# Kernel tuning notes

Hardware: AMD Instinct MI355X
Metric: run time of the kernel (lower is better)

Reference implementation:

```python
import jax, jax.numpy as jnp
import numpy as np

E, H, K = 8, 256, 2        # num_experts, hidden_size, top-k
B, S, TD, ID = 16, 1024, 768, 1024
EPS = 1e-5

def gelu(x):
    return jax.nn.gelu(x, approximate=False)  # torch nn.GELU default = exact erf

def layer_norm(x, g, b):
    m = jnp.mean(x, axis=-1, keepdims=True)
    v = jnp.var(x, axis=-1, keepdims=True)
    return (x - m) * jax.lax.rsqrt(v + EPS) * g + b

def moe(x, gate_W, gate_b, W1, b1, W2, b2):
    # x: [B,S,H]
    gates = jax.nn.softmax(x @ gate_W + gate_b, axis=-1)        # [B,S,E]
    topv, topi = jax.lax.top_k(gates, K)                        # [B,S,K]
    # dense all-expert compute (faithful to the torch loop+stack)
    h = gelu(jnp.einsum('bsh,ehg->bseg', x, W1) + b1)           # [B,S,E,H]
    eo = jnp.einsum('bseg,egh->bseh', h, W2) + b2               # [B,S,E,H]
    sel = jnp.take_along_axis(eo, topi[..., None], axis=2)      # [B,S,K,H]
    return jnp.sum(sel * topv[..., None], axis=2)               # [B,S,H]

def setup_inputs() -> dict:
    key = jax.random.key(0)
    ks = jax.random.split(key, 12)
    def n(k, shape, scale=0.05):
        return jax.random.normal(k, shape, jnp.float32) * scale
    return dict(
        x=jax.random.normal(ks[0], (B, S, TD), jnp.float32),
        We=n(ks[1], (TD, H)), be=jnp.zeros((H,), jnp.float32),
        l2_emb=n(ks[2], (H,)), cl_emb=n(ks[3], (H,)),
        gate_W=n(ks[4], (H, E)), gate_b=jnp.zeros((E,), jnp.float32),
        W1=n(ks[5], (E, H, H)), b1=jnp.zeros((E, H), jnp.float32),
        W2=n(ks[6], (E, H, H)), b2=jnp.zeros((E, H), jnp.float32),
        l2_g=jnp.ones((H,), jnp.float32), l2_b=jnp.zeros((H,), jnp.float32),
        cl_g=jnp.ones((H,), jnp.float32), cl_b=jnp.zeros((H,), jnp.float32),
        Wt2i=n(ks[7], (H, ID)), bt2i=jnp.zeros((ID,), jnp.float32),
        Wcl=n(ks[8], (H, H)), bcl=jnp.zeros((H,), jnp.float32),
    )

def reference(x, We, be, l2_emb, cl_emb, gate_W, gate_b, W1, b1, W2, b2,
              l2_g, l2_b, cl_g, cl_b, Wt2i, bt2i, Wcl, bcl):
    # task == 'text2image'
    x = gelu(x @ We + be)                                       # text_embed + gelu
    l2_in = x + l2_emb
    cl_in = x + cl_emb
    l2 = gelu(layer_norm(moe(l2_in, gate_W, gate_b, W1, b1, W2, b2), l2_g, l2_b)) + l2_in
    cl = gelu(layer_norm(moe(cl_in, gate_W, gate_b, W1, b1, W2, b2), cl_g, cl_b)) + cl_in
    l2_res = l2 @ Wt2i + bt2i                                   # text_to_image head
    cl_res = cl @ Wcl + bcl                                     # cl_text_to_image head
    return (l2_res, cl_res)
```

## Files before the change

### kernel.cpp

```cpp
#include <hip/hip_runtime.h>
#include <hip/hip_bf16.h>
#include <math.h>

typedef __bf16 bf16_t;
typedef __bf16 bf16x4 __attribute__((ext_vector_type(4)));
typedef __bf16 bf16x8 __attribute__((ext_vector_type(8)));
typedef float  f32x4  __attribute__((ext_vector_type(4)));

#define NTOK 16384
#define HD   256
#define TD   768
#define ID   1024
#define NPAIR 32768
#define MOE_TPB 520
#define FLAG_CAP 4096

__device__ inline float fast_erf(float x){
    float ax = fabsf(x);
    float t = 1.0f / (1.0f + 0.3275911f*ax);
    float y = t*(0.254829592f + t*(-0.284496736f + t*(1.421413741f +
              t*(-1.453152027f + t*1.061405429f))));
    float e = 1.0f - y*__expf(-ax*ax);
    return copysignf(e, x);
}
__device__ inline float gelu_f(float x){
    return 0.5f * x * (1.0f + fast_erf(x * 0.70710678118654752f));
}
__device__ inline bf16x4 cvt4(float4 a){
    bf16x4 o; o[0]=(bf16_t)a.x; o[1]=(bf16_t)a.y; o[2]=(bf16_t)a.z; o[3]=(bf16_t)a.w; return o;
}
__device__ inline f32x4 mfma16(bf16x8 a, bf16x8 b, f32x4 c){
    return __builtin_amdgcn_mfma_f32_16x16x32_bf16(a, b, c, 0, 0, 0);
}

__global__ void k_zero(int* meta){
    if (threadIdx.x < 64) meta[threadIdx.x] = 0;
}

__global__ __launch_bounds__(256) void k_convert(
    const float* __restrict__ We, const float* __restrict__ W1,
    const float* __restrict__ W2, const float* __restrict__ Wt,
    const float* __restrict__ Wc,
    bf16_t* __restrict__ WeHi, bf16_t* __restrict__ WeLo,
    bf16_t* __restrict__ W1T,
    bf16_t* __restrict__ W2T, bf16_t* __restrict__ WtT, bf16_t* __restrict__ WcT)
{
    int idx = blockIdx.x*256 + threadIdx.x;
    if (idx < 196608){ int n=idx/768, k=idx%768; float f = We[k*256+n];
        bf16_t h = (bf16_t)f; WeHi[idx] = h; WeLo[idx] = (bf16_t)(f - (float)h); return; }
    idx -= 196608;
    if (idx < 524288){ int e=idx>>16, r=idx&65535, n=r>>8, k=r&255;
        W1T[(e<<16)+(n<<8)+k] = (bf16_t)W1[(e<<16)+(k<<8)+n]; return; }
    idx -= 524288;
    if (idx < 524288){ int e=idx>>16, r=idx&65535, n=r>>8, k=r&255;
        W2T[(e<<16)+(n<<8)+k] = (bf16_t)W2[(e<<16)+(k<<8)+n]; return; }
    idx -= 524288;
    if (idx < 262144){ int n=idx>>8, k=idx&255; WtT[idx] = (bf16_t)Wt[k*1024+n]; return; }
    idx -= 262144;
    if (idx < 65536){ int n=idx>>8, k=idx&255; WcT[idx] = (bf16_t)Wc[k*256+n]; return; }
}

__global__ __launch_bounds__(256) void k_embed(
    const float* __restrict__ x, const bf16_t* __restrict__ WeHi,
    const bf16_t* __restrict__ WeLo,
    const float* __restrict__ be, const float* __restrict__ l2e,
    const float* __restrict__ cle,
    float* __restrict__ l2f, float* __restrict__ clf)
{
    __shared__ bf16_t Ah[128][40];
    __shared__ bf16_t Al[128][40];
    __shared__ bf16_t Bh[64][40];
    __shared__ bf16_t Bl[64][40];
    int row0 = blockIdx.x*128, col0 = blockIdx.y*64;
    int t = threadIdx.x, wave = t>>6, lane = t&63;
    int wm = wave>>1, wn = wave&1;
    f32x4 acc[4][2] = {};
    for (int k0 = 0; k0 < TD; k0 += 32){
        __syncthreads();
        #pragma unroll
        for (int u=0; u<4; ++u){
            int fi = u*256 + t, r = fi>>3, q = fi&7;
            float4 v = *(const float4*)(x + (size_t)(row0+r)*TD + k0 + q*4);
            bf16x4 h = cvt4(v);
            float4 rl;
            rl.x = v.x-(float)h[0]; rl.y = v.y-(float)h[1];
            rl.z = v.z-(float)h[2]; rl.w = v.w-(float)h[3];
            *(bf16x4*)(&Ah[r][q*4]) = h;
            *(bf16x4*)(&Al[r][q*4]) = cvt4(rl);
        }
        {
            int r = t>>2, q = t&3;
            *(bf16x8*)(&Bh[r][q*8]) = *(const bf16x8*)(WeHi + (size_t)(col0+r)*TD + k0 + q*8);
            *(bf16x8*)(&Bl[r][q*8]) = *(const bf16x8*)(WeLo + (size_t)(col0+r)*TD + k0 + q*8);
        }
        __syncthreads();
        int kq = lane>>4, lr = lane&15;
        bf16x8 ah[4], al[4], bh[2], bl[2];
        #pragma unroll
        for (int m=0;m<4;++m){
            ah[m] = *(const bf16x8*)(&Ah[wm*64 + m*16 + lr][kq*8]);
            al[m] = *(const bf16x8*)(&Al[wm*64 + m*16 + lr][kq*8]);
        }
        #pragma unroll
        for (int n=0;n<2;++n){
            bh[n] = *(const bf16x8*)(&Bh[wn*32 + n*16 + lr][kq*8]);
            bl[n] = *(const bf16x8*)(&Bl[wn*32 + n*16 + lr][kq*8]);
        }
        #pragma unroll
        for (int m=0;m<4;++m)
            #pragma unroll
            for (int n=0;n<2;++n){
                acc[m][n] = mfma16(ah[m], bh[n], acc[m][n]);
                acc[m][n] = mfma16(ah[m], bl[n], acc[m][n]);
                acc[m][n] = mfma16(al[m], bh[n], acc[m][n]);
            }
    }
    int kq = lane>>4, lr = lane&15;
    #pragma unroll
    for (int n=0;n<2;++n){
        int col = col0 + wn*32 + n*16 + lr;
        float bv = be[col], lv = l2e[col], cv = cle[col];
        #pragma unroll
        for (int m=0;m<4;++m)
            #pragma unroll
            for (int r=0;r<4;++r){
                int row = row0 + wm*64 + m*16 + kq*4 + r;
                float v = gelu_f(acc[m][n][r] + bv);
                l2f[(size_t)row*HD + col] = v + lv;
                clf[(size_t)row*HD + col] = v + cv;
            }
    }
}

__global__ __launch_bounds__(256) void k_gate(
    const float* __restrict__ l2f, const float* __restrict__ clf,
    const float* __restrict__ gW, const float* __restrict__ gb,
    float* __restrict__ topv, int* __restrict__ topi,
    int* __restrict__ flaglist, int* __restrict__ nflag,
    bf16_t* __restrict__ l2h, bf16_t* __restrict__ clh)
{
    __shared__ float gw[2048];
    int t = threadIdx.x;
    for (int i=t; i<2048; i+=256) gw[i] = gW[i];
    __syncthreads();
    int wave = t>>6, lane = t&63;
    int idx = blockIdx.x*4 + wave;
    int br = idx>>14, tok = idx&16383;
    const float* in = br ? clf : l2f;
    float4 v = *(const float4*)(in + (size_t)tok*HD + lane*4);
    float xv[4] = {v.x, v.y, v.z, v.w};
    {
        bf16x4 hv; hv[0]=(bf16_t)v.x; hv[1]=(bf16_t)v.y; hv[2]=(bf16_t)v.z; hv[3]=(bf16_t)v.w;
        bf16_t* hout = br ? clh : l2h;
        *(bf16x4*)(hout + (size_t)tok*HD + lane*4) = hv;
    }
    float p[8];
    #pragma unroll
    for (int e=0;e<8;++e) p[e] = 0.f;
    #pragma unroll
    for (int j=0;j<4;++j){
        const float* g = &gw[(lane*4+j)*8];
        #pragma unroll
        for (int e=0;e<8;++e) p[e] += xv[j]*g[e];
    }
    #pragma unroll
    for (int e=0;e<8;++e){
        float s = p[e];
        #pragma unroll
        for (int o=32;o>0;o>>=1) s += __shfl_xor(s, o);
        p[e] = s + gb[e];
    }
    float mx = p[0];
    #pragma unroll
    for (int e=1;e<8;++e) mx = fmaxf(mx, p[e]);
    float den = 0.f;
    #pragma unroll
    for (int e=0;e<8;++e) den += expf(p[e]-mx);
    int i1 = 0; float m1 = p[0];
    #pragma unroll
    for (int e=1;e<8;++e) if (p[e] > m1){ m1 = p[e]; i1 = e; }
    int i2 = (i1==0)?1:0; float m2 = p[i2];
    #pragma unroll
    for (int e=0;e<8;++e) if (e != i1 && p[e] > m2){ m2 = p[e]; i2 = e; }
    if (lane == 0){
        topv[idx*2]   = expf(m1-mx)/den;
        topv[idx*2+1] = expf(m2-mx)/den;
        topi[idx*2]   = i1;
        topi[idx*2+1] = i2;
        float m3 = -1e30f;
        #pragma unroll
        for (int e=0;e<8;++e) if (e != i1 && e != i2) m3 = fmaxf(m3, p[e]);
        if (m2 - m3 < 1e-3f){
            int slot = atomicAdd(nflag, 1);
            if (slot < FLAG_CAP) flaglist[slot] = idx;
        }
    }
}

__global__ __launch_bounds__(256) void k_refine(
    const float* __restrict__ x, const float* __restrict__ We,
    const float* __restrict__ be,
    const float* __restrict__ l2e, const float* __restrict__ cle,
    const float* __restrict__ gW, const float* __restrict__ gb,
    const int* __restrict__ flaglist, const int* __restrict__ nflag,
    float* __restrict__ topv, int* __restrict__ topi)
{
    __shared__ float xs[768];
    __shared__ double red[256][8];
    int t = threadIdx.x;
    int nf = *nflag; if (nf > FLAG_CAP) nf = FLAG_CAP;
    for (int f = blockIdx.x; f < nf; f += gridDim.x){
        int idx = flaglist[f];
        int br = idx>>14, tok = idx&16383;
        __syncthreads();
        for (int i=t; i<768; i+=256) xs[i] = x[(size_t)tok*768 + i];
        __syncthreads();
        double u = 0.0;
        for (int j=0;j<768;++j) u += (double)xs[j] * (double)We[(size_t)j*256 + t];
        u += (double)be[t];
        double act = 0.5*u*(1.0 + erf(u*0.70710678118654752440));
        double li = act + (double)(br ? cle[t] : l2e[t]);
        #pragma unroll
        for (int e=0;e<8;++e) red[t][e] = li * (double)gW[t*8+e];
        __syncthreads();
        for (int s=128; s>0; s>>=1){
            if (t < s){
                #pragma unroll
                for (int e=0;e<8;++e) red[t][e] += red[t+s][e];
            }
            __syncthreads();
        }
        if (t == 0){
            double p[8];
            #pragma unroll
            for (int e=0;e<8;++e) p[e] = red[0][e] + (double)gb[e];
            int i1 = 0; double m1 = p[0];
            #pragma unroll
            for (int e=1;e<8;++e) if (p[e] > m1){ m1 = p[e]; i1 = e; }
            int i2 = (i1==0)?1:0; double m2 = p[i2];
            #pragma unroll
            for (int e=0;e<8;++e) if (e != i1 && p[e] > m2){ m2 = p[e]; i2 = e; }
            double mx = m1, den = 0.0;
            #pragma unroll
            for (int e=0;e<8;++e) den += exp(p[e]-mx);
            topv[idx*2]   = (float)(exp(m1-mx)/den);
            topv[idx*2+1] = (float)(exp(m2-mx)/den);
            topi[idx*2]   = i1;
            topi[idx*2+1] = i2;
        }
    }
}

__global__ __launch_bounds__(256) void k_hist(
    const int* __restrict__ topi, int* __restrict__ blockhist)
{
    __shared__ int h[16];
    int t = threadIdx.x;
    if (t < 16) h[t] = 0;
    __syncthreads();
    int idx = blockIdx.x*256 + t;
    int br = idx>>14;
    atomicAdd(&h[br*8 + topi[idx*2]], 1);
    atomicAdd(&h[br*8 + topi[idx*2+1]], 1);
    __syncthreads();
    if (t < 16) blockhist[blockIdx.x*16 + t] = h[t];
}

__global__ void k_scan(const int* __restrict__ blockhist, int* __restrict__ base,
                       int4* __restrict__ table)
{
    __shared__ int tot[16], off[16], tpre[2][9];
    int t = threadIdx.x;
    if (t < 16){
        int s = 0;
        for (int b=0;b<128;++b){ base[b*16+t] = s; s += blockhist[b*16+t]; }
        tot[t] = s;
    }
    __syncthreads();
    if (t == 0){
        for (int br=0;br<2;++br){
            int s=0, tp=0; tpre[br][0]=0;
            for (int e=0;e<8;++e){
                off[br*8+e]=s; s += tot[br*8+e];
                tp += (tot[br*8+e]+63)>>6; tpre[br][e+1]=tp;
            }
        }
    }
    __syncthreads();
    for (int i=t; i<2048; i+=256) base[i] += off[i&15];
    for (int i=t; i<2*MOE_TPB; i+=256){
        int b = i/MOE_TPB, ti = i%MOE_TPB;
        int4 ent = make_int4(-1,0,0,0);
        if (ti < tpre[b][8]){
            int e = 0;
            while (ti >= tpre[b][e+1]) ++e;
            int k = ti - tpre[b][e];
            int s = off[b*8+e] + k*64;
            int en = off[b*8+e] + tot[b*8+e];
            ent = make_int4(e, s, (s+64 < en) ? (s+64) : en, b);
        }
        table[i] = ent;
    }
}

__global__ __launch_bounds__(256) void k_scatter(
    const int* __restrict__ topi, const int* __restrict__ base,
    int* __restrict__ rows, int* __restrict__ posof)
{
    __shared__ int h[16];
    int t = threadIdx.x;
    if (t < 16) h[t] = 0;
    __syncthreads();
    int idx = blockIdx.x*256 + t;
    int br = idx>>14, tok = idx&16383;
    int e0 = topi[idx*2], e1 = topi[idx*2+1];
    int r0 = atomicAdd(&h[br*8+e0], 1);
    int r1 = atomicAdd(&h[br*8+e1], 1);
    int p0 = base[blockIdx.x*16 + br*8 + e0] + r0;
    int p1 = base[blockIdx.x*16 + br*8 + e1] + r1;
    rows[br*NPAIR + p0] = tok;
    rows[br*NPAIR + p1] = tok;
    posof[idx*2]   = p0;
    posof[idx*2+1] = p1;
}

__global__ __launch_bounds__(512, 4) void k_moe(
    const int4* __restrict__ table, const int* __restrict__ rows,
    const bf16_t* __restrict__ l2h, const bf16_t* __restrict__ clh,
    const bf16_t* __restrict__ W1T, const bf16_t* __restrict__ W2T,
    const float* __restrict__ b1, const float* __restrict__ b2,
    bf16_t* __restrict__ eo)
{
    int4 te = table[blockIdx.x];
    int e = te.x, start = te.y, end = te.z, br = te.w;
    if (e < 0) return;
    const bf16_t* inb = br ? clh : l2h;

    __shared__ bf16_t Hs[64*256];
    char* hb = (char*)Hs;

    int t = threadIdx.x, w = t>>6, lane = t&63;
    int wm = w>>2, wn = w&3;
    int kq = lane>>4, lr = lane&15;

    int rowoff[2];
    #pragma unroll
    for (int m=0;m<2;++m){
        int pos = start + wm*32 + m*16 + lr;
        int tok = rows[br*NPAIR + ((pos < end) ? pos : start)];
        rowoff[m] = tok*HD + kq*8;
    }
    const bf16_t* b1p = W1T + ((size_t)e<<16) + (size_t)(wn*64 + lr)*HD + kq*8;
    f32x4 acc[2][4] = {};
    #pragma unroll
    for (int k0=0;k0<8;++k0){
        bf16x8 af[2], bfr[4];
        #pragma unroll
        for (int m=0;m<2;++m) af[m] = *(const bf16x8*)(inb + rowoff[m] + k0*32);
        #pragma unroll
        for (int n=0;n<4;++n) bfr[n] = *(const bf16x8*)(b1p + (size_t)(n*16)*HD + k0*32);
        #pragma unroll
        for (int m=0;m<2;++m)
            #pragma unroll
            for (int n=0;n<4;++n) acc[m][n] = mfma16(af[m], bfr[n], acc[m][n]);
    }
    #pragma unroll
    for (int n=0;n<4;++n){
        int col = wn*64 + n*16 + lr;
        float bv = b1[e*256 + col];
        #pragma unroll
        for (int m=0;m<2;++m)
            #pragma unroll
            for (int r=0;r<4;++r){
                int row = wm*32 + m*16 + kq*4 + r;
                int byte = row*512 + ((((col>>3) ^ (row&7))<<4)) + (col&7)*2;
                *(bf16_t*)(hb + byte) = (bf16_t)gelu_f(acc[m][n][r] + bv);
            }
    }
    __syncthreads();
    #pragma unroll
    for (int m=0;m<2;++m)
        #pragma unroll
        for (int n=0;n<4;++n)
            #pragma unroll
            for (int r=0;r<4;++r) acc[m][n][r] = 0.f;
    const bf16_t* b2p = W2T + ((size_t)e<<16) + (size_t)(wn*64 + lr)*HD + kq*8;
    #pragma unroll
    for (int k0=0;k0<8;++k0){
        bf16x8 af[2], bfr[4];
        #pragma unroll
        for (int m=0;m<2;++m){
            int row = wm*32 + m*16 + lr;
            af[m] = *(const bf16x8*)(hb + row*512 + (((k0*4 + kq) ^ (row&7))<<4));
        }
        #pragma unroll
        for (int n=0;n<4;++n) bfr[n] = *(const bf16x8*)(b2p + (size_t)(n*16)*HD + k0*32);
        #pragma unroll
        for (int m=0;m<2;++m)
            #pragma unroll
            for (int n=0;n<4;++n) acc[m][n] = mfma16(af[m], bfr[n], acc[m][n]);
    }
    __syncthreads();
    #pragma unroll
    for (int n=0;n<4;++n){
        int col = wn*64 + n*16 + lr;
        float bv = b2[e*256 + col];
        #pragma unroll
        for (int m=0;m<2;++m)
            #pragma unroll
            for (int r=0;r<4;++r){
                int row = wm*32 + m*16 + kq*4 + r;
                int byte = row*512 + ((((col>>3) ^ (row&7))<<4)) + (col&7)*2;
                *(bf16_t*)(hb + byte) = (bf16_t)(acc[m][n][r] + bv);
            }
    }
    __syncthreads();
    #pragma unroll
    for (int i=0;i<4;++i){
        int c = i*512 + t;
        int row = c>>5, cir = c&31;
        bf16x8 v = *(const bf16x8*)(hb + row*512 + ((cir ^ (row&7))<<4));
        int pos = start + row;
        if (pos < end)
            *(bf16x8*)(eo + ((size_t)br*NPAIR + pos)*HD + cir*8) = v;
    }
}

__global__ __launch_bounds__(256) void k_combine(
    const bf16_t* __restrict__ eo, const float* __restrict__ topv,
    const int* __restrict__ posof,
    const float* __restrict__ l2f, const float* __restrict__ clf,
    const float* __restrict__ l2g, const float* __restrict__ l2b,
    const float* __restrict__ clg, const float* __restrict__ clb,
    bf16_t* __restrict__ yl2, bf16_t* __restrict__ ycl)
{
    int t = threadIdx.x, wave = t>>6, lane = t&63;
    int idx = blockIdx.x*4 + wave;
    int br = idx>>14, tok = idx&16383;
    const float* in = br ? clf : l2f;
    const float* g  = br ? clg : l2g;
    const float* bb = br ? clb : l2b;
    bf16_t* y = br ? ycl : yl2;
    int p0 = posof[idx*2], p1 = posof[idx*2+1];
    float w0 = topv[idx*2], w1 = topv[idx*2+1];
    bf16x4 e0 = *(const bf16x4*)(eo + ((size_t)br*NPAIR + p0)*HD + lane*4);
    bf16x4 e1 = *(const bf16x4*)(eo + ((size_t)br*NPAIR + p1)*HD + lane*4);
    float v[4], s = 0.f, s2 = 0.f;
    #pragma unroll
    for (int j=0;j<4;++j){
        v[j] = w0*(float)e0[j] + w1*(float)e1[j];
        s += v[j]; s2 += v[j]*v[j];
    }
    #pragma unroll
    for (int o=32;o>0;o>>=1){ s += __shfl_xor(s, o); s2 += __shfl_xor(s2, o); }
    float mean = s * (1.f/256.f);
    float var  = s2 * (1.f/256.f) - mean*mean;
    float inv  = rsqrtf(var + 1e-5f);
    float4 iv = *(const float4*)(in + (size_t)tok*HD + lane*4);
    float ivv[4] = {iv.x, iv.y, iv.z, iv.w};
    bf16x4 ov;
    #pragma unroll
    for (int j=0;j<4;++j){
        int c = lane*4 + j;
        float ln = (v[j]-mean)*inv*g[c] + bb[c];
        ov[j] = (bf16_t)(gelu_f(ln) + ivv[j]);
    }
    *(bf16x4*)(y + (size_t)tok*HD + lane*4) = ov;
}

__global__ __launch_bounds__(256) void k_head(
    const bf16_t* __restrict__ A, const bf16_t* __restrict__ BT,
    const float* __restrict__ bias, float* __restrict__ out, int Nout)
{
    __shared__ bf16_t As[128][40];
    __shared__ bf16_t Bs[64][40];
    int row0 = blockIdx.x*128, col0 = blockIdx.y*64;
    int t = threadIdx.x, wave = t>>6, lane = t&63;
    int wm = wave>>1, wn = wave&1;
    f32x4 acc[4][2] = {};
    for (int k0=0; k0<HD; k0+=32){
        __syncthreads();
        #pragma unroll
        for (int u=0;u<2;++u){
            int fi = u*256 + t, r = fi>>2, q = fi&3;
            *(bf16x8*)(&As[r][q*8]) = *(const bf16x8*)(A + (size_t)(row0+r)*HD + k0 + q*8);
        }
        {
            int r = t>>2, q = t&3;
            *(bf16x8*)(&Bs[r][q*8]) = *(const bf16x8*)(BT + (size_t)(col0+r)*HD + k0 + q*8);
        }
        __syncthreads();
        int kq = lane>>4, lr = lane&15;
        bf16x8 af[4], bfr[2];
        #pragma unroll
        for (int m=0;m<4;++m) af[m] = *(const bf16x8*)(&As[wm*64 + m*16 + lr][kq*8]);
        #pragma unroll
        for (int n=0;n<2;++n) bfr[n] = *(const bf16x8*)(&Bs[wn*32 + n*16 + lr][kq*8]);
        #pragma unroll
        for (int m=0;m<4;++m)
            #pragma unroll
            for (int n=0;n<2;++n) acc[m][n] = mfma16(af[m], bfr[n], acc[m][n]);
    }
    int kq = lane>>4, lr = lane&15;
    #pragma unroll
    for (int n=0;n<2;++n){
        int col = col0 + wn*32 + n*16 + lr;
        float bv = bias[col];
        #pragma unroll
        for (int m=0;m<4;++m)
            #pragma unroll
            for (int r=0;r<4;++r){
                int row = row0 + wm*64 + m*16 + kq*4 + r;
                out[(size_t)row*Nout + col] = acc[m][n][r] + bv;
            }
    }
}

extern "C" void kernel_launch(void* const* d_in, const int* in_sizes, int n_in,
                              void* d_out, int out_size, void* d_ws, size_t ws_size,
                              hipStream_t stream)
{
    const float* x   = (const float*)d_in[0];
    const float* We  = (const float*)d_in[1];
    const float* be  = (const float*)d_in[2];
    const float* l2e = (const float*)d_in[3];
    const float* cle = (const float*)d_in[4];
    const float* gW  = (const float*)d_in[5];
    const float* gb  = (const float*)d_in[6];
    const float* W1  = (const float*)d_in[7];
    const float* b1  = (const float*)d_in[8];
    const float* W2  = (const float*)d_in[9];
    const float* b2  = (const float*)d_in[10];
    const float* l2g = (const float*)d_in[11];
    const float* l2b = (const float*)d_in[12];
    const float* clg = (const float*)d_in[13];
    const float* clb = (const float*)d_in[14];
    const float* Wt  = (const float*)d_in[15];
    const float* bt  = (const float*)d_in[16];
    const float* Wcl = (const float*)d_in[17];
    const float* bcl = (const float*)d_in[18];
    float* out = (float*)d_out;
    char* ws = (char*)d_ws;

    const size_t O_META  = 0;
    const size_t O_TABLE = 256;
    const size_t O_TOPV  = 17152;
    const size_t O_TOPI  = 279296;
    const size_t O_POSOF = 541440;
    const size_t O_ROWS  = 803584;
    const size_t O_WEHI  = 1065728;
    const size_t O_W1T   = 1458944;
    const size_t O_W2T   = 2507520;
    const size_t O_WTT   = 3556096;
    const size_t O_WCLT  = 4080384;
    const size_t O_L2F   = 4211456;
    const size_t O_CLF   = 20988672;
    const size_t O_EO    = 37765888;
    const size_t O_L2H   = 71320320;
    const size_t O_CLH   = 79708928;
    const size_t O_WELO  = 88097536;
    const size_t O_FLAG  = 88490752;
    const size_t O_BASE  = 88507136;
    const size_t O_BH    = 88515328;
    const size_t NEED    = 88523520;
    if (ws_size < NEED) return;

    int*    meta    = (int*)(ws + O_META);
    int*    nflag   = meta + 48;
    int4*   table   = (int4*)(ws + O_TABLE);
    int*    blockhist = (int*)(ws + O_BH);
    float*  topv    = (float*)(ws + O_TOPV);
    int*    topi    = (int*)(ws + O_TOPI);
    int*    posof   = (int*)(ws + O_POSOF);
    int*    rows    = (int*)(ws + O_ROWS);
    bf16_t* WeHi    = (bf16_t*)(ws + O_WEHI);
    bf16_t* WeLo    = (bf16_t*)(ws + O_WELO);
    int*    flaglist= (int*)(ws + O_FLAG);
    int*    basep   = (int*)(ws + O_BASE);
    bf16_t* W1T     = (bf16_t*)(ws + O_W1T);
    bf16_t* W2T     = (bf16_t*)(ws + O_W2T);
    bf16_t* WtT     = (bf16_t*)(ws + O_WTT);
    bf16_t* WcT     = (bf16_t*)(ws + O_WCLT);
    float*  l2f     = (float*)(ws + O_L2F);
    float*  clf     = (float*)(ws + O_CLF);
    bf16_t* eo      = (bf16_t*)(ws + O_EO);
    bf16_t* l2h     = (bf16_t*)(ws + O_L2H);
    bf16_t* clh     = (bf16_t*)(ws + O_CLH);
    bf16_t* yl2     = (bf16_t*)(ws + O_L2H);
    bf16_t* ycl     = (bf16_t*)(ws + O_CLH);

    k_zero<<<1, 64, 0, stream>>>(meta);
    k_convert<<<6144, 256, 0, stream>>>(We, W1, W2, Wt, Wcl, WeHi, WeLo, W1T, W2T, WtT, WcT);
    k_embed<<<dim3(128,4), 256, 0, stream>>>(x, WeHi, WeLo, be, l2e, cle, l2f, clf);
    k_gate<<<8192, 256, 0, stream>>>(l2f, clf, gW, gb, topv, topi, flaglist, nflag, l2h, clh);
    k_refine<<<256, 256, 0, stream>>>(x, We, be, l2e, cle, gW, gb, flaglist, nflag, topv, topi);
    k_hist<<<128, 256, 0, stream>>>(topi, blockhist);
    k_scan<<<1, 256, 0, stream>>>(blockhist, basep, table);
    k_scatter<<<128, 256, 0, stream>>>(topi, basep, rows, posof);
    k_moe<<<2*MOE_TPB, 512, 0, stream>>>(table, rows, l2h, clh, W1T, W2T, b1, b2, eo);
    k_combine<<<8192, 256, 0, stream>>>(eo, topv, posof, l2f, clf, l2g, l2b, clg, clb, yl2, ycl);
    k_head<<<dim3(128,16), 256, 0, stream>>>(yl2, WtT, bt, out, 1024);
    k_head<<<dim3(128,4), 256, 0, stream>>>(ycl, WcT, bcl, out + (size_t)16777216, 256);
}
```

Baseline: 267.6 us.

## Stage MoE operands into LDS via direct global-to-LDS loads; tile weight transpose

The MoE expert kernel now loads token activations and chunks of the expert weight matrices straight into shared memory with global_load_lds, using a swizzled layout. MFMA fragments then read from LDS instead of directly from global memory. The final store writes scalar bf16 outputs directly, skipping the LDS round-trip. The weight convert kernel is rewritten as a 64x64 tiled transpose through shared memory for coalesced reads and writes. This adds barriers and doubles shared memory per block, which may lower occupancy and serialize loads against compute.

```diff
diff --git a/kernel.cpp b/kernel.cpp
--- a/kernel.cpp
+++ b/kernel.cpp
@@ -32,6 +32,11 @@
 __device__ inline f32x4 mfma16(bf16x8 a, bf16x8 b, f32x4 c){
     return __builtin_amdgcn_mfma_f32_16x16x32_bf16(a, b, c, 0, 0, 0);
 }
+__device__ inline void gload_lds16(const void* g, void* l){
+    __builtin_amdgcn_global_load_lds(
+        (const __attribute__((address_space(1))) unsigned int*)g,
+        (__attribute__((address_space(3))) unsigned int*)l, 16, 0, 0);
+}
 
 __global__ void k_zero(int* meta){
     if (threadIdx.x < 64) meta[threadIdx.x] = 0;
@@ -45,19 +50,46 @@
     bf16_t* __restrict__ W1T,
     bf16_t* __restrict__ W2T, bf16_t* __restrict__ WtT, bf16_t* __restrict__ WcT)
 {
-    int idx = blockIdx.x*256 + threadIdx.x;
-    if (idx < 196608){ int n=idx/768, k=idx%768; float f = We[k*256+n];
-        bf16_t h = (bf16_t)f; WeHi[idx] = h; WeLo[idx] = (bf16_t)(f - (float)h); return; }
-    idx -= 196608;
-    if (idx < 524288){ int e=idx>>16, r=idx&65535, n=r>>8, k=r&255;
-        W1T[(e<<16)+(n<<8)+k] = (bf16_t)W1[(e<<16)+(k<<8)+n]; return; }
-    idx -= 524288;
-    if (idx < 524288){ int e=idx>>16, r=idx&65535, n=r>>8, k=r&255;
-        W2T[(e<<16)+(n<<8)+k] = (bf16_t)W2[(e<<16)+(k<<8)+n]; return; }
-    idx -= 524288;
-    if (idx < 262144){ int n=idx>>8, k=idx&255; WtT[idx] = (bf16_t)Wt[k*1024+n]; return; }
-    idx -= 262144;
-    if (idx < 65536){ int n=idx>>8, k=idx&255; WcT[idx] = (bf16_t)Wc[k*256+n]; return; }
+    __shared__ float T[64][65];
+    int job = blockIdx.x;
+    const float* src; bf16_t* dst; bf16_t* dst2 = nullptr;
+    int K, N, k0, n0;
+    if (job < 48){ src = We;  dst = WeHi; dst2 = WeLo; K = 768; N = 256;
+        k0 = (job>>2)*64; n0 = (job&3)*64;
+    } else if (job < 176){ int e = (job-48)>>4, tj = (job-48)&15;
+        src = W1 + ((size_t)e<<16); dst = W1T + ((size_t)e<<16); K=256; N=256;
+        k0 = (tj>>2)*64; n0 = (tj&3)*64;
+    } else if (job < 304){ int e = (job-176)>>4, tj = (job-176)&15;
+        src = W2 + ((size_t)e<<16); dst = W2T + ((size_t)e<<16); K=256; N=256;
+        k0 = (tj>>2)*64; n0 = (tj&3)*64;
+    } else if (job < 368){ int tj = job-304; src = Wt; dst = WtT; K=256; N=1024;
+        k0 = (tj>>4)*64; n0 = (tj&15)*64;
+    } else { int tj = job-368; src = Wc; dst = WcT; K=256; N=256;
+        k0 = (tj>>2)*64; n0 = (tj&3)*64;
+    }
+    int t = threadIdx.x;
+    #pragma unroll
+    for (int u=0;u<4;++u){
+        int unit = u*256 + t;
+        int r = unit>>4, c4 = (unit&15)*4;
+        float4 v = *(const float4*)(src + (size_t)(k0+r)*N + n0 + c4);
+        T[r][c4] = v.x; T[r][c4+1] = v.y; T[r][c4+2] = v.z; T[r][c4+3] = v.w;
+    }
+    __syncthreads();
+    #pragma unroll
+    for (int u=0;u<4;++u){
+        int unit = u*256 + t;
+        int rn = unit>>4, c4 = (unit&15)*4;
+        bf16x4 h, l;
+        #pragma unroll
+        for (int j=0;j<4;++j){
+            float f = T[c4+j][rn];
+            bf16_t hb = (bf16_t)f;
+            h[j] = hb; l[j] = (bf16_t)(f - (float)hb);
+        }
+        *(bf16x4*)(dst + (size_t)(n0+rn)*K + k0 + c4) = h;
+        if (dst2) *(bf16x4*)(dst2 + (size_t)(n0+rn)*K + k0 + c4) = l;
+    }
 }
 
 __global__ __launch_bounds__(256) void k_embed(
@@ -336,33 +368,72 @@
     if (e < 0) return;
     const bf16_t* inb = br ? clh : l2h;
 
-    __shared__ bf16_t Hs[64*256];
-    char* hb = (char*)Hs;
+    __shared__ bf16_t Ab[64*256];
+    __shared__ bf16_t Bb[256*64];
+    char* ab = (char*)Ab;
+    char* bb = (char*)Bb;
 
     int t = threadIdx.x, w = t>>6, lane = t&63;
     int wm = w>>2, wn = w&3;
     int kq = lane>>4, lr = lane&15;
 
-    int rowoff[2];
-    #pragma unroll
-    for (int m=0;m<2;++m){
-        int pos = start + wm*32 + m*16 + lr;
+    #pragma unroll
+    for (int u=0; u<4; ++u){
+        int unit = (w*4+u)*64 + lane;
+        int row = unit>>5, ch = unit&31;
+        int pos = start + row;
         int tok = rows[br*NPAIR + ((pos < end) ? pos : start)];
-        rowoff[m] = tok*HD + kq*8;
-    }
-    const bf16_t* b1p = W1T + ((size_t)e<<16) + (size_t)(wn*64 + lr)*HD + kq*8;
+        gload_lds16(inb + (size_t)tok*HD + ((ch ^ (row&7))<<3), ab + (w*4+u)*1024);
+    }
+    const bf16_t* W1e = W1T + ((size_t)e<<16);
+    const bf16_t* W2e = W2T + ((size_t)e<<16);
+    #pragma unroll
+    for (int u=0; u<4; ++u){
+        int unit = (w*4+u)*64 + lane;
+        int row = unit>>3, c = unit&7;
+        gload_lds16(W1e + (size_t)row*HD + ((c ^ (row&7))<<3), bb + (w*4+u)*1024);
+    }
+    __syncthreads();
+
     f32x4 acc[2][4] = {};
-    #pragma unroll
-    for (int k0=0;k0<8;++k0){
-        bf16x8 af[2], bfr[4];
-        #pragma unroll
-        for (int m=0;m<2;++m) af[m] = *(const bf16x8*)(inb + rowoff[m] + k0*32);
-        #pragma unroll
-        for (int n=0;n<4;++n) bfr[n] = *(const bf16x8*)(b1p + (size_t)(n*16)*HD + k0*32);
-        #pragma unroll
-        for (int m=0;m<2;++m)
-            #pragma unroll
-            for (int n=0;n<4;++n) acc[m][n] = mfma16(af[m], bfr[n], acc[m][n]);
+    for (int s=0; s<4; ++s){
+        #pragma unroll
+        for (int kk=0; kk<2; ++kk){
+            bf16x8 af[2], bfr[4];
+            #pragma unroll
+            for (int m=0;m<2;++m){
+                int row = wm*32 + m*16 + lr;
+                int ch = s*8 + kk*4 + kq;
+                af[m] = *(const bf16x8*)(ab + row*512 + ((ch ^ (row&7))<<4));
+            }
+            #pragma unroll
+            for (int n=0;n<4;++n){
+                int nc = wn*64 + n*16 + lr;
+                int c = kk*4 + kq;
+                bfr[n] = *(const bf16x8*)(bb + nc*128 + ((c ^ (nc&7))<<4));
+            }
+            #pragma unroll
+            for (int m=0;m<2;++m)
+                #pragma unroll
+                for (int n=0;n<4;++n) acc[m][n] = mfma16(af[m], bfr[n], acc[m][n]);
+        }
+        __syncthreads();
+        if (s < 3){
+            #pragma unroll
+            for (int u=0; u<4; ++u){
+                int unit = (w*4+u)*64 + lane;
+                int row = unit>>3, c = unit&7;
+                gload_lds16(W1e + (size_t)row*HD + (s+1)*64 + ((c ^ (row&7))<<3),
+                            bb + (w*4+u)*1024);
+            }
+            __syncthreads();
+        }
+    }
+    #pragma unroll
+    for (int u=0; u<4; ++u){
+        int unit = (w*4+u)*64 + lane;
+        int row = unit>>3, c = unit&7;
+        gload_lds16(W2e + (size_t)row*HD + ((c ^ (row&7))<<3), bb + (w*4+u)*1024);
     }
     #pragma unroll
     for (int n=0;n<4;++n){
@@ -374,7 +445,7 @@
             for (int r=0;r<4;++r){
                 int row = wm*32 + m*16 + kq*4 + r;
                 int byte = row*512 + ((((col>>3) ^ (row&7))<<4)) + (col&7)*2;
-                *(bf16_t*)(hb + byte) = (bf16_t)gelu_f(acc[m][n][r] + bv);
+                *(bf16_t*)(ab + byte) = (bf16_t)gelu_f(acc[m][n][r] + bv);
             }
     }
     __syncthreads();
@@ -384,23 +455,39 @@
         for (int n=0;n<4;++n)
             #pragma unroll
             for (int r=0;r<4;++r) acc[m][n][r] = 0.f;
-    const bf16_t* b2p = W2T + ((size_t)e<<16) + (size_t)(wn*64 + lr)*HD + kq*8;
-    #pragma unroll
-    for (int k0=0;k0<8;++k0){
-        bf16x8 af[2], bfr[4];
-        #pragma unroll
-        for (int m=0;m<2;++m){
-            int row = wm*32 + m*16 + lr;
-            af[m] = *(const bf16x8*)(hb + row*512 + (((k0*4 + kq) ^ (row&7))<<4));
-        }
-        #pragma unroll
-        for (int n=0;n<4;++n) bfr[n] = *(const bf16x8*)(b2p + (size_t)(n*16)*HD + k0*32);
-        #pragma unroll
-        for (int m=0;m<2;++m)
-            #pragma unroll
-            for (int n=0;n<4;++n) acc[m][n] = mfma16(af[m], bfr[n], acc[m][n]);
-    }
-    __syncthreads();
+    for (int s=0; s<4; ++s){
+        #pragma unroll
+        for (int kk=0; kk<2; ++kk){
+            bf16x8 af[2], bfr[4];
+            #pragma unroll
+            for (int m=0;m<2;++m){
+                int row = wm*32 + m*16 + lr;
+                int ch = s*8 + kk*4 + kq;
+                af[m] = *(const bf16x8*)(ab + row*512 + ((ch ^ (row&7))<<4));
+            }
+            #pragma unroll
+            for (int n=0;n<4;++n){
+                int nc = wn*64 + n*16 + lr;
+                int c = kk*4 + kq;
+                bfr[n] = *(const bf16x8*)(bb + nc*128 + ((c ^ (nc&7))<<4));
+            }
+            #pragma unroll
+            for (int m=0;m<2;++m)
+                #pragma unroll
+                for (int n=0;n<4;++n) acc[m][n] = mfma16(af[m], bfr[n], acc[m][n]);
+        }
+        if (s < 3){
+            __syncthreads();
+            #pragma unroll
+            for (int u=0; u<4; ++u){
+                int unit = (w*4+u)*64 + lane;
+                int row = unit>>3, c = unit&7;
+                gload_lds16(W2e + (size_t)row*HD + (s+1)*64 + ((c ^ (row&7))<<3),
+                            bb + (w*4+u)*1024);
+            }
+            __syncthreads();
+        }
+    }
     #pragma unroll
     for (int n=0;n<4;++n){
         int col = wn*64 + n*16 + lr;
@@ -409,20 +496,10 @@
         for (int m=0;m<2;++m)
             #pragma unroll
             for (int r=0;r<4;++r){
-                int row = wm*32 + m*16 + kq*4 + r;
-                int byte = row*512 + ((((col>>3) ^ (row&7))<<4)) + (col&7)*2;
-                *(bf16_t*)(hb + byte) = (bf16_t)(acc[m][n][r] + bv);
-            }
-    }
-    __syncthreads();
-    #pragma unroll
-    for (int i=0;i<4;++i){
-        int c = i*512 + t;
-        int row = c>>5, cir = c&31;
-        bf16x8 v = *(const bf16x8*)(hb + row*512 + ((cir ^ (row&7))<<4));
-        int pos = start + row;
-        if (pos < end)
-            *(bf16x8*)(eo + ((size_t)br*NPAIR + pos)*HD + cir*8) = v;
+                int pos = start + wm*32 + m*16 + kq*4 + r;
+                if (pos < end)
+                    eo[((size_t)br*NPAIR + pos)*HD + col] = (bf16_t)(acc[m][n][r] + bv);
+            }
     }
 }
 
@@ -590,7 +667,7 @@
     bf16_t* ycl     = (bf16_t*)(ws + O_CLH);
 
     k_zero<<<1, 64, 0, stream>>>(meta);
-    k_convert<<<6144, 256, 0, stream>>>(We, W1, W2, Wt, Wcl, WeHi, WeLo, W1T, W2T, WtT, WcT);
+    k_convert<<<384, 256, 0, stream>>>(We, W1, W2, Wt, Wcl, WeHi, WeLo, W1T, W2T, WtT, WcT);
     k_embed<<<dim3(128,4), 256, 0, stream>>>(x, WeHi, WeLo, be, l2e, cle, l2f, clf);
     k_gate<<<8192, 256, 0, stream>>>(l2f, clf, gW, gb, topv, topi, flaglist, nflag, l2h, clh);
     k_refine<<<256, 256, 0, stream>>>(x, We, be, l2e, cle, gW, gb, flaglist, nflag, topv, topi);
```

Measured after the change: 217.2 us. 18.8% less time.
